# Optimization experiments

Hardware: AMD Instinct MI355X
Metric: run time of the kernel (lower is better)

The kernel has to match this reference:

```python
import jax, jax.numpy as jnp
import numpy as np

DIM = 768
NUM_HEADS = 8
GROUPS = 2


def setup_inputs() -> dict:
    key = jax.random.key(0)
    ks = jax.random.split(key, 6)
    B, N, C = 8, 1024, DIM
    x = jax.random.normal(ks[0], (B, N, C), dtype=jnp.float32)
    # nn.Linear weights stored (out_features, in_features), applied as x @ W.T
    w_qkv = jax.random.normal(ks[1], (3 * C, C), dtype=jnp.float32) * 0.02
    g_dim = C // GROUPS
    w_g0 = jax.random.normal(ks[2], (3 * g_dim, g_dim), dtype=jnp.float32) * 0.02
    w_g1 = jax.random.normal(ks[3], (3 * g_dim, g_dim), dtype=jnp.float32) * 0.02
    w_proj = jax.random.normal(ks[4], (C, C), dtype=jnp.float32) * 0.02
    b_proj = jax.random.normal(ks[5], (C,), dtype=jnp.float32) * 0.02
    return {"x": x, "w_qkv": w_qkv, "w_g0": w_g0, "w_g1": w_g1,
            "w_proj": w_proj, "b_proj": b_proj}


def reference(x, w_qkv, w_g0, w_g1, w_proj, b_proj):
    B, N, C = x.shape
    H = NUM_HEADS
    hd = C // H
    scale = hd ** (-0.5)  # qk_scale=None -> head_dim^-0.5, reused in group attn
    g = GROUPS
    g_dim = C // g

    # ---- standard MHSA branch ----
    qkv = (x @ w_qkv.T).reshape(B, N, 3, H, hd)
    qkv = jnp.transpose(qkv, (2, 0, 3, 1, 4))  # (3, B, H, N, hd)
    q, k, v = qkv[0], qkv[1], qkv[2]
    attn = jax.nn.softmax(jnp.einsum('bhnd,bhmd->bhnm', q, k) * scale, axis=-1)
    origin = jnp.einsum('bhnm,bhmd->bhnd', attn, v)  # (B, H, N, hd)
    origin = origin.swapaxes(1, 2).reshape(B, N, g, g_dim)

    # ---- sequential per-group head-fusion branch ----
    xg = x.reshape(B, N, g, g_dim)
    head_x = jnp.zeros((B, N, g_dim), dtype=x.dtype)
    outputs = []
    for i, w in enumerate([w_g0, w_g1]):  # fixed small loop, g=2
        cur = xg[:, :, i] + head_x
        qkv2 = (cur @ w.T).reshape(B, N, 3, g_dim)
        q2, k2, v2 = qkv2[:, :, 0], qkv2[:, :, 1], qkv2[:, :, 2]
        a2 = jax.nn.softmax(jnp.einsum('bnd,bmd->bnm', q2, k2) * scale, axis=-1)
        head_x = jnp.einsum('bnm,bmd->bnd', a2, v2)
        outputs.append(head_x + origin[:, :, i])

    out = jnp.concatenate(outputs, axis=-1)
    return out @ w_proj.T + b_proj
```

## Files before the change

### kernel.cpp

```cpp
#include <hip/hip_runtime.h>
#include <cstdint>
#include <cstddef>

#define DEV_INLINE __device__ __forceinline__

typedef __bf16 bf16;
typedef __bf16 bf16x8 __attribute__((ext_vector_type(8)));
typedef float f32x4 __attribute__((ext_vector_type(4)));

static constexpr int Bb = 8;
static constexpr int Nn = 1024;
static constexpr int Cc = 768;
static constexpr int HD = 96;
static constexpr int GD = 384;
#define SCALE_ 0.1020620726159658f

DEV_INLINE void gload_lds16(void* lds, const void* g) {
  __builtin_amdgcn_global_load_lds(
      (__attribute__((address_space(1))) void*)(void*)g,
      (__attribute__((address_space(3))) void*)lds, 16, 0, 0);
}

__global__ void k_f32_to_bf16(const float* __restrict__ src, bf16* __restrict__ dst, int n) {
  int i = (blockIdx.x * 256 + threadIdx.x) * 8;
  if (i >= n) return;
  float4 a = *(const float4*)(src + i);
  float4 b = *(const float4*)(src + i + 4);
  bf16x8 o;
  o[0] = (bf16)a.x; o[1] = (bf16)a.y; o[2] = (bf16)a.z; o[3] = (bf16)a.w;
  o[4] = (bf16)b.x; o[5] = (bf16)b.y; o[6] = (bf16)b.z; o[7] = (bf16)b.w;
  *(bf16x8*)(dst + i) = o;
}

__global__ void k_make_cur(const float* __restrict__ x, const float* __restrict__ hx,
                           bf16* __restrict__ cur, int gi) {
  int t = blockIdx.x * 256 + threadIdx.x;
  int m = t / 48;
  int d0 = (t % 48) * 8;
  const float* xr = x + (size_t)m * Cc + gi * GD + d0;
  float4 a = *(const float4*)xr;
  float4 b = *(const float4*)(xr + 4);
  if (gi) {
    const float* hr = hx + (size_t)m * GD + d0;
    float4 c = *(const float4*)hr;
    float4 d = *(const float4*)(hr + 4);
    a.x += c.x; a.y += c.y; a.z += c.z; a.w += c.w;
    b.x += d.x; b.y += d.y; b.z += d.z; b.w += d.w;
  }
  bf16x8 o;
  o[0] = (bf16)a.x; o[1] = (bf16)a.y; o[2] = (bf16)a.z; o[3] = (bf16)a.w;
  o[4] = (bf16)b.x; o[5] = (bf16)b.y; o[6] = (bf16)b.z; o[7] = (bf16)b.w;
  *(bf16x8*)(cur + (size_t)m * GD + d0) = o;
}

template <int EPI>
__global__ __launch_bounds__(256, 2)
void k_gemm(const bf16* __restrict__ A, const bf16* __restrict__ W, int K,
            int aZ, int wZ,
            bf16* __restrict__ o0, bf16* __restrict__ o1, bf16* __restrict__ o2,
            float* __restrict__ f0, const float* __restrict__ bias,
            const float* __restrict__ origin, int gi) {
  const int bm = blockIdx.x, bn = blockIdx.y, bz = blockIdx.z;
  const int tid = threadIdx.x;
  const int wave = tid >> 6, lane = tid & 63;
  const int wr = wave >> 1, wc = wave & 1;
  const int l15 = lane & 15, l4 = lane >> 4;

  A += (size_t)bz * aZ;
  W += (size_t)bz * wZ;

  __shared__ bf16 As[128 * 32];
  __shared__ bf16 Bs[128 * 32];

  f32x4 acc[4][4] = {};

  const int t8 = tid * 8;
  const int r0 = t8 >> 5, c0 = t8 & 31;
  const int r1 = r0 + 64;
  const bf16* Arow0 = A + (size_t)(bm * 128 + r0) * K + c0;
  const bf16* Arow1 = A + (size_t)(bm * 128 + r1) * K + c0;
  const bf16* Brow0 = W + (size_t)(bn * 128 + r0) * K + c0;
  const bf16* Brow1 = W + (size_t)(bn * 128 + r1) * K + c0;
  bf16* sA0 = &As[wave * 512];
  bf16* sA1 = &As[2048 + wave * 512];
  bf16* sB0 = &Bs[wave * 512];
  bf16* sB1 = &Bs[2048 + wave * 512];

  for (int k0 = 0; k0 < K; k0 += 32) {
    gload_lds16(sA0, Arow0 + k0);
    gload_lds16(sA1, Arow1 + k0);
    gload_lds16(sB0, Brow0 + k0);
    gload_lds16(sB1, Brow1 + k0);
    __syncthreads();
    bf16x8 af[4], bfr[4];
#pragma unroll
    for (int i = 0; i < 4; ++i) {
      af[i]  = *(const bf16x8*)&As[(wr * 64 + i * 16 + l15) * 32 + l4 * 8];
      bfr[i] = *(const bf16x8*)&Bs[(wc * 64 + i * 16 + l15) * 32 + l4 * 8];
    }
#pragma unroll
    for (int i = 0; i < 4; ++i)
#pragma unroll
      for (int j = 0; j < 4; ++j)
        acc[i][j] = __builtin_amdgcn_mfma_f32_16x16x32_bf16(af[i], bfr[j], acc[i][j], 0, 0, 0);
    __syncthreads();
  }

#pragma unroll
  for (int i = 0; i < 4; ++i) {
    const int mbase = bm * 128 + wr * 64 + i * 16 + l4 * 4;
#pragma unroll
    for (int j = 0; j < 4; ++j) {
      const int col = bn * 128 + wc * 64 + j * 16 + l15;
#pragma unroll
      for (int r = 0; r < 4; ++r) {
        const int row = mbase + r;
        const float val = acc[i][j][r];
        if constexpr (EPI == 2) {
          f0[(size_t)row * 768 + col] = val + bias[col];
        } else if constexpr (EPI == 3) {
          o0[((size_t)bz * 1024 + row) * 1024 + col] = (bf16)(val * SCALE_);
        } else if constexpr (EPI == 4) {
          const size_t gr = (size_t)bz * 1024 + row;
          f0[gr * 384 + col] = val;
          const size_t ci = gr * 768 + gi * 384 + col;
          o1[ci] = (bf16)(val + origin[ci]);
        } else if constexpr (EPI == 0) {
          const int bb = row >> 10, n = row & 1023;
          const int sct = col / 768, rem = col % 768;
          const int hh = rem / 96, dd = rem % 96;
          const bf16 bv = (bf16)val;
          if (sct == 0)      o0[((size_t)(bb * 8 + hh) * 1024 + n) * 96 + dd] = bv;
          else if (sct == 1) o1[((size_t)(bb * 8 + hh) * 1024 + n) * 96 + dd] = bv;
          else               o2[((size_t)(bb * 8 + hh) * 96 + dd) * 1024 + n] = bv;
        } else {
          const int bb = row >> 10, n = row & 1023;
          const int sct = col / 384, dd = col % 384;
          const bf16 bv = (bf16)val;
          if (sct == 0)      o0[(size_t)row * 384 + dd] = bv;
          else if (sct == 1) o1[(size_t)row * 384 + dd] = bv;
          else               o2[((size_t)bb * 384 + dd) * 1024 + n] = bv;
        }
      }
    }
  }
}

__global__ __launch_bounds__(256)
void k_softmax_rows(bf16* __restrict__ SP) {
  const int row = blockIdx.x * 4 + (threadIdx.x >> 6);
  const int lane = threadIdx.x & 63;
  bf16* R = SP + (size_t)row * 1024 + lane * 16;
  bf16x8 a = *(const bf16x8*)R;
  bf16x8 b = *(const bf16x8*)(R + 8);
  float v[16];
#pragma unroll
  for (int i = 0; i < 8; ++i) { v[i] = (float)a[i]; v[8 + i] = (float)b[i]; }
  float mx = -1e30f;
#pragma unroll
  for (int i = 0; i < 16; ++i) mx = fmaxf(mx, v[i]);
  mx = fmaxf(mx, __shfl_xor(mx, 1));
  mx = fmaxf(mx, __shfl_xor(mx, 2));
  mx = fmaxf(mx, __shfl_xor(mx, 4));
  mx = fmaxf(mx, __shfl_xor(mx, 8));
  mx = fmaxf(mx, __shfl_xor(mx, 16));
  mx = fmaxf(mx, __shfl_xor(mx, 32));
  float s = 0.f;
#pragma unroll
  for (int i = 0; i < 16; ++i) { v[i] = __expf(v[i] - mx); s += v[i]; }
  s += __shfl_xor(s, 1);
  s += __shfl_xor(s, 2);
  s += __shfl_xor(s, 4);
  s += __shfl_xor(s, 8);
  s += __shfl_xor(s, 16);
  s += __shfl_xor(s, 32);
  const float inv = 1.f / s;
#pragma unroll
  for (int i = 0; i < 8; ++i) { a[i] = (bf16)(v[i] * inv); b[i] = (bf16)(v[8 + i] * inv); }
  *(bf16x8*)R = a;
  *(bf16x8*)(R + 8) = b;
}

__global__ __launch_bounds__(256, 2)
void k_flash_mha(const bf16* __restrict__ Q, const bf16* __restrict__ Kt,
                 const bf16* __restrict__ Vt, float* __restrict__ origin) {
  const int bh = blockIdx.x, qb = blockIdx.y;
  const int b = bh >> 3, h = bh & 7;
  const int wave = threadIdx.x >> 6, lane = threadIdx.x & 63;
  const int l15 = lane & 15, l4 = lane >> 4;
  const bf16* Qh = Q + (size_t)bh * Nn * HD;
  const bf16* Kh = Kt + (size_t)bh * Nn * HD;
  const bf16* Vh = Vt + (size_t)bh * HD * Nn;
  const int q0 = qb * 128 + wave * 32;

  bf16x8 qf[2][3];
#pragma unroll
  for (int mf = 0; mf < 2; ++mf)
#pragma unroll
    for (int kf = 0; kf < 3; ++kf)
      qf[mf][kf] = *(const bf16x8*)&Qh[(size_t)(q0 + mf * 16 + l15) * HD + kf * 32 + l4 * 8];

  f32x4 o[2][6] = {};
  float mrow[2][4], lrow[2][4];
#pragma unroll
  for (int mf = 0; mf < 2; ++mf)
#pragma unroll
    for (int r = 0; r < 4; ++r) { mrow[mf][r] = -1e30f; lrow[mf][r] = 0.f; }

  __shared__ bf16 Plds[4][32 * 88];
  bf16* Pl = &Plds[wave][0];

  for (int n0 = 0; n0 < Nn; n0 += 64) {
    f32x4 s[2][4] = {};
#pragma unroll
    for (int nf = 0; nf < 4; ++nf)
#pragma unroll
      for (int kf = 0; kf < 3; ++kf) {
        bf16x8 kfr = *(const bf16x8*)&Kh[(size_t)(n0 + nf * 16 + l15) * HD + kf * 32 + l4 * 8];
#pragma unroll
        for (int mf = 0; mf < 2; ++mf)
          s[mf][nf] = __builtin_amdgcn_mfma_f32_16x16x32_bf16(qf[mf][kf], kfr, s[mf][nf], 0, 0, 0);
      }
#pragma unroll
    for (int mf = 0; mf < 2; ++mf)
#pragma unroll
      for (int r = 0; r < 4; ++r) {
        float mx = -1e30f;
#pragma unroll
        for (int nf = 0; nf < 4; ++nf) {
          s[mf][nf][r] *= SCALE_;
          mx = fmaxf(mx, s[mf][nf][r]);
        }
        mx = fmaxf(mx, __shfl_xor(mx, 1));
        mx = fmaxf(mx, __shfl_xor(mx, 2));
        mx = fmaxf(mx, __shfl_xor(mx, 4));
        mx = fmaxf(mx, __shfl_xor(mx, 8));
        float mnew = fmaxf(mrow[mf][r], mx);
        float alpha = __expf(mrow[mf][r] - mnew);
        mrow[mf][r] = mnew;
        float ls = 0.f;
#pragma unroll
        for (int nf = 0; nf < 4; ++nf) {
          float p = __expf(s[mf][nf][r] - mnew);
          s[mf][nf][r] = p;
          ls += p;
        }
        ls += __shfl_xor(ls, 1); ls += __shfl_xor(ls, 2);
        ls += __shfl_xor(ls, 4); ls += __shfl_xor(ls, 8);
        lrow[mf][r] = lrow[mf][r] * alpha + ls;
#pragma unroll
        for (int df = 0; df < 6; ++df) o[mf][df][r] *= alpha;
      }
#pragma unroll
    for (int mf = 0; mf < 2; ++mf)
#pragma unroll
      for (int nf = 0; nf < 4; ++nf)
#pragma unroll
        for (int r = 0; r < 4; ++r)
          Pl[(mf * 16 + l4 * 4 + r) * 88 + nf * 16 + l15] = (bf16)s[mf][nf][r];
    bf16x8 pa[2][2];
#pragma unroll
    for (int mf = 0; mf < 2; ++mf)
#pragma unroll
      for (int kf2 = 0; kf2 < 2; ++kf2)
        pa[mf][kf2] = *(const bf16x8*)&Pl[(mf * 16 + l15) * 88 + kf2 * 32 + l4 * 8];
#pragma unroll
    for (int df = 0; df < 6; ++df)
#pragma unroll
      for (int kf2 = 0; kf2 < 2; ++kf2) {
        bf16x8 vf = *(const bf16x8*)&Vh[(size_t)(df * 16 + l15) * Nn + n0 + kf2 * 32 + l4 * 8];
#pragma unroll
        for (int mf = 0; mf < 2; ++mf)
          o[mf][df] = __builtin_amdgcn_mfma_f32_16x16x32_bf16(pa[mf][kf2], vf, o[mf][df], 0, 0, 0);
      }
  }

  float* Og = origin + (size_t)b * Nn * Cc + h * HD;
#pragma unroll
  for (int mf = 0; mf < 2; ++mf)
#pragma unroll
    for (int r = 0; r < 4; ++r) {
      const int row = q0 + mf * 16 + l4 * 4 + r;
      const float inv = 1.f / lrow[mf][r];
#pragma unroll
      for (int df = 0; df < 6; ++df)
        Og[(size_t)row * Cc + df * 16 + l15] = o[mf][df][r] * inv;
    }
}

extern "C" void kernel_launch(void* const* d_in, const int* in_sizes, int n_in,
                              void* d_out, int out_size, void* d_ws, size_t ws_size,
                              hipStream_t stream) {
  const float* x      = (const float*)d_in[0];
  const float* w_qkv  = (const float*)d_in[1];
  const float* w_g0   = (const float*)d_in[2];
  const float* w_g1   = (const float*)d_in[3];
  const float* w_proj = (const float*)d_in[4];
  const float* b_proj = (const float*)d_in[5];
  float* out = (float*)d_out;

  char* ws = (char*)d_ws;
  size_t off = 0;
  auto alloc = [&](size_t bytes) {
    char* p = ws + off;
    off += (bytes + 255) & ~(size_t)255;
    return p;
  };
  bf16* xb     = (bf16*)alloc((size_t)8192 * 768 * 2);
  bf16* wqkvb  = (bf16*)alloc((size_t)2304 * 768 * 2);
  bf16* wg0b   = (bf16*)alloc((size_t)1152 * 384 * 2);
  bf16* wg1b   = (bf16*)alloc((size_t)1152 * 384 * 2);
  bf16* wprojb = (bf16*)alloc((size_t)768 * 768 * 2);
  float* origin = (float*)alloc((size_t)8192 * 768 * 4);
  char* R = alloc((size_t)67108864);
  bf16* Qb = (bf16*)R;
  bf16* Kb = (bf16*)(R + 12582912);
  bf16* Vt = (bf16*)(R + 25165824);
  bf16* curb = (bf16*)R;
  bf16* q2   = (bf16*)(R + 6291456);
  bf16* k2   = (bf16*)(R + 12582912);
  bf16* v2t  = (bf16*)(R + 18874368);
  float* hx  = (float*)(R + 25165824);
  bf16* cat  = (bf16*)(R + 37748736);
  bf16* SP   = (bf16*)(R + 50331648);

  k_f32_to_bf16<<<dim3(3072), 256, 0, stream>>>(x, xb, 8192 * 768);
  k_f32_to_bf16<<<dim3(864), 256, 0, stream>>>(w_qkv, wqkvb, 2304 * 768);
  k_f32_to_bf16<<<dim3(216), 256, 0, stream>>>(w_g0, wg0b, 1152 * 384);
  k_f32_to_bf16<<<dim3(216), 256, 0, stream>>>(w_g1, wg1b, 1152 * 384);
  k_f32_to_bf16<<<dim3(288), 256, 0, stream>>>(w_proj, wprojb, 768 * 768);

  k_gemm<0><<<dim3(64, 18), 256, 0, stream>>>(xb, wqkvb, 768, 0, 0, Qb, Kb, Vt, nullptr, nullptr, nullptr, 0);
  k_flash_mha<<<dim3(64, 8), 256, 0, stream>>>(Qb, Kb, Vt, origin);

  for (int gi = 0; gi < 2; ++gi) {
    const bf16* wg = gi ? wg1b : wg0b;
    k_make_cur<<<dim3(1536), 256, 0, stream>>>(x, hx, curb, gi);
    k_gemm<1><<<dim3(64, 9), 256, 0, stream>>>(curb, wg, 384, 0, 0, q2, k2, v2t, nullptr, nullptr, nullptr, 0);
    k_gemm<3><<<dim3(8, 8, 8), 256, 0, stream>>>(q2, k2, 384, 1024 * 384, 1024 * 384,
                                                 SP, nullptr, nullptr, nullptr, nullptr, nullptr, 0);
    k_softmax_rows<<<dim3(2048), 256, 0, stream>>>(SP);
    k_gemm<4><<<dim3(8, 3, 8), 256, 0, stream>>>(SP, v2t, 1024, 1024 * 1024, 384 * 1024,
                                                 nullptr, cat, nullptr, hx, nullptr, origin, gi);
  }

  k_gemm<2><<<dim3(64, 6), 256, 0, stream>>>(cat, wprojb, 768, 0, 0, nullptr, nullptr, nullptr, out, b_proj, nullptr, 0);
}
```

Baseline: 448.8 us.

## Double-buffer K/V tiles in LDS for flash MHA and fuse conversion kernels

```diff
diff --git a/kernel.cpp b/kernel.cpp
--- a/kernel.cpp
+++ b/kernel.cpp
@@ -5,6 +5,7 @@
 #define DEV_INLINE __device__ __forceinline__
 
 typedef __bf16 bf16;
+typedef __bf16 bf16x4 __attribute__((ext_vector_type(4)));
 typedef __bf16 bf16x8 __attribute__((ext_vector_type(8)));
 typedef float f32x4 __attribute__((ext_vector_type(4)));
 
@@ -21,15 +22,25 @@
       (__attribute__((address_space(3))) void*)lds, 16, 0, 0);
 }
 
-__global__ void k_f32_to_bf16(const float* __restrict__ src, bf16* __restrict__ dst, int n) {
-  int i = (blockIdx.x * 256 + threadIdx.x) * 8;
-  if (i >= n) return;
-  float4 a = *(const float4*)(src + i);
-  float4 b = *(const float4*)(src + i + 4);
+__global__ void k_convert_all(const float* __restrict__ x, const float* __restrict__ wqkv,
+                              const float* __restrict__ wg0, const float* __restrict__ wg1,
+                              const float* __restrict__ wproj,
+                              bf16* __restrict__ xb, bf16* __restrict__ wqkvb,
+                              bf16* __restrict__ wg0b, bf16* __restrict__ wg1b,
+                              bf16* __restrict__ wprojb) {
+  const int i = (blockIdx.x * 256 + threadIdx.x) * 8;
+  const float* src; bf16* dst; int off;
+  if (i < 6291456)      { src = x;     dst = xb;     off = i; }
+  else if (i < 8060928) { src = wqkv;  dst = wqkvb;  off = i - 6291456; }
+  else if (i < 8503296) { src = wg0;   dst = wg0b;   off = i - 8060928; }
+  else if (i < 8945664) { src = wg1;   dst = wg1b;   off = i - 8503296; }
+  else                  { src = wproj; dst = wprojb; off = i - 8945664; }
+  float4 a = *(const float4*)(src + off);
+  float4 b = *(const float4*)(src + off + 4);
   bf16x8 o;
   o[0] = (bf16)a.x; o[1] = (bf16)a.y; o[2] = (bf16)a.z; o[3] = (bf16)a.w;
   o[4] = (bf16)b.x; o[5] = (bf16)b.y; o[6] = (bf16)b.z; o[7] = (bf16)b.w;
-  *(bf16x8*)(dst + i) = o;
+  *(bf16x8*)(dst + off) = o;
 }
 
 __global__ void k_make_cur(const float* __restrict__ x, const float* __restrict__ hx,
@@ -193,6 +204,13 @@
   const bf16* Vh = Vt + (size_t)bh * HD * Nn;
   const int q0 = qb * 128 + wave * 32;
 
+  __shared__ bf16 Ks[2][64 * 96];
+  __shared__ bf16 Vs[2][96 * 64];
+  __shared__ bf16 Plds[4][32 * 88];
+  __shared__ float aux[4][32];
+  bf16* Pl = &Plds[wave][0];
+  float* Ax = &aux[wave][0];
+
   bf16x8 qf[2][3];
 #pragma unroll
   for (int mf = 0; mf < 2; ++mf)
@@ -201,63 +219,101 @@
       qf[mf][kf] = *(const bf16x8*)&Qh[(size_t)(q0 + mf * 16 + l15) * HD + kf * 32 + l4 * 8];
 
   f32x4 o[2][6] = {};
-  float mrow[2][4], lrow[2][4];
-#pragma unroll
-  for (int mf = 0; mf < 2; ++mf)
-#pragma unroll
-    for (int r = 0; r < 4; ++r) { mrow[mf][r] = -1e30f; lrow[mf][r] = 0.f; }
-
-  __shared__ bf16 Plds[4][32 * 88];
-  bf16* Pl = &Plds[wave][0];
-
-  for (int n0 = 0; n0 < Nn; n0 += 64) {
+  float mrow[2] = {-1e30f, -1e30f}, lrow[2] = {0.f, 0.f};
+
+  auto stageK = [&](int buf, int n0) {
+#pragma unroll
+    for (int i = 0; i < 3; ++i) {
+      const int c = i * 4 + wave;
+      gload_lds16(&Ks[buf][c * 512], Kh + (size_t)n0 * 96 + c * 512 + lane * 8);
+    }
+  };
+  auto stageV = [&](int buf, int n0) {
+#pragma unroll
+    for (int i = 0; i < 3; ++i) {
+      const int c = i * 4 + wave;
+      const int L = (c * 64 + lane) * 16;
+      const int row = L >> 7;
+      const int colb = (L & 127) ^ ((row & 7) << 4);
+      gload_lds16(&Vs[buf][c * 512], Vh + (size_t)row * Nn + n0 + (colb >> 1));
+    }
+  };
+
+  auto compute = [&](int buf) {
     f32x4 s[2][4] = {};
 #pragma unroll
-    for (int nf = 0; nf < 4; ++nf)
-#pragma unroll
-      for (int kf = 0; kf < 3; ++kf) {
-        bf16x8 kfr = *(const bf16x8*)&Kh[(size_t)(n0 + nf * 16 + l15) * HD + kf * 32 + l4 * 8];
+    for (int nf = 0; nf < 4; ++nf) {
+      bf16x8 kfr[3];
+#pragma unroll
+      for (int kf = 0; kf < 3; ++kf)
+        kfr[kf] = *(const bf16x8*)&Ks[buf][(nf * 16 + l15) * 96 + kf * 32 + l4 * 8];
+#pragma unroll
+      for (int kf = 0; kf < 3; ++kf)
 #pragma unroll
         for (int mf = 0; mf < 2; ++mf)
-          s[mf][nf] = __builtin_amdgcn_mfma_f32_16x16x32_bf16(qf[mf][kf], kfr, s[mf][nf], 0, 0, 0);
-      }
-#pragma unroll
-    for (int mf = 0; mf < 2; ++mf)
-#pragma unroll
-      for (int r = 0; r < 4; ++r) {
-        float mx = -1e30f;
-#pragma unroll
-        for (int nf = 0; nf < 4; ++nf) {
+          s[mf][nf] = __builtin_amdgcn_mfma_f32_16x16x32_bf16(kfr[kf], qf[mf][kf], s[mf][nf], 0, 0, 0);
+    }
+    float pmax[2];
+#pragma unroll
+    for (int mf = 0; mf < 2; ++mf) {
+      float mx = -1e30f;
+#pragma unroll
+      for (int nf = 0; nf < 4; ++nf)
+#pragma unroll
+        for (int r = 0; r < 4; ++r) {
           s[mf][nf][r] *= SCALE_;
           mx = fmaxf(mx, s[mf][nf][r]);
         }
-        mx = fmaxf(mx, __shfl_xor(mx, 1));
-        mx = fmaxf(mx, __shfl_xor(mx, 2));
-        mx = fmaxf(mx, __shfl_xor(mx, 4));
-        mx = fmaxf(mx, __shfl_xor(mx, 8));
-        float mnew = fmaxf(mrow[mf][r], mx);
-        float alpha = __expf(mrow[mf][r] - mnew);
-        mrow[mf][r] = mnew;
-        float ls = 0.f;
-#pragma unroll
-        for (int nf = 0; nf < 4; ++nf) {
-          float p = __expf(s[mf][nf][r] - mnew);
+      mx = fmaxf(mx, __shfl_xor(mx, 16));
+      mx = fmaxf(mx, __shfl_xor(mx, 32));
+      pmax[mf] = mx;
+    }
+    const bool need = (pmax[0] > mrow[0] + 8.f) || (pmax[1] > mrow[1] + 8.f);
+    if (__any(need)) {
+#pragma unroll
+      for (int mf = 0; mf < 2; ++mf) {
+        const float mnew = fmaxf(mrow[mf], pmax[mf]);
+        const float alpha = __expf(mrow[mf] - mnew);
+        mrow[mf] = mnew;
+        lrow[mf] *= alpha;
+        if (l4 == 0) Ax[mf * 16 + l15] = alpha;
+      }
+      float ar[2][4];
+#pragma unroll
+      for (int mf = 0; mf < 2; ++mf)
+#pragma unroll
+        for (int r = 0; r < 4; ++r) ar[mf][r] = Ax[mf * 16 + l4 * 4 + r];
+#pragma unroll
+      for (int mf = 0; mf < 2; ++mf)
+#pragma unroll
+        for (int df = 0; df < 6; ++df)
+#pragma unroll
+          for (int r = 0; r < 4; ++r) o[mf][df][r] *= ar[mf][r];
+    }
+#pragma unroll
+    for (int mf = 0; mf < 2; ++mf) {
+      float ls = 0.f;
+#pragma unroll
+      for (int nf = 0; nf < 4; ++nf)
+#pragma unroll
+        for (int r = 0; r < 4; ++r) {
+          const float p = __expf(s[mf][nf][r] - mrow[mf]);
           s[mf][nf][r] = p;
           ls += p;
         }
-        ls += __shfl_xor(ls, 1); ls += __shfl_xor(ls, 2);
-        ls += __shfl_xor(ls, 4); ls += __shfl_xor(ls, 8);
-        lrow[mf][r] = lrow[mf][r] * alpha + ls;
-#pragma unroll
-        for (int df = 0; df < 6; ++df) o[mf][df][r] *= alpha;
+      ls += __shfl_xor(ls, 16);
+      ls += __shfl_xor(ls, 32);
+      lrow[mf] += ls;
+    }
+#pragma unroll
+    for (int mf = 0; mf < 2; ++mf)
+#pragma unroll
+      for (int nf = 0; nf < 4; ++nf) {
+        bf16x4 pk;
+        pk[0] = (bf16)s[mf][nf][0]; pk[1] = (bf16)s[mf][nf][1];
+        pk[2] = (bf16)s[mf][nf][2]; pk[3] = (bf16)s[mf][nf][3];
+        *(bf16x4*)&Pl[(mf * 16 + l15) * 88 + nf * 16 + l4 * 4] = pk;
       }
-#pragma unroll
-    for (int mf = 0; mf < 2; ++mf)
-#pragma unroll
-      for (int nf = 0; nf < 4; ++nf)
-#pragma unroll
-        for (int r = 0; r < 4; ++r)
-          Pl[(mf * 16 + l4 * 4 + r) * 88 + nf * 16 + l15] = (bf16)s[mf][nf][r];
     bf16x8 pa[2][2];
 #pragma unroll
     for (int mf = 0; mf < 2; ++mf)
@@ -265,26 +321,53 @@
       for (int kf2 = 0; kf2 < 2; ++kf2)
         pa[mf][kf2] = *(const bf16x8*)&Pl[(mf * 16 + l15) * 88 + kf2 * 32 + l4 * 8];
 #pragma unroll
-    for (int df = 0; df < 6; ++df)
+    for (int df = 0; df < 6; ++df) {
+      bf16x8 vfr[2];
 #pragma unroll
       for (int kf2 = 0; kf2 < 2; ++kf2) {
-        bf16x8 vf = *(const bf16x8*)&Vh[(size_t)(df * 16 + l15) * Nn + n0 + kf2 * 32 + l4 * 8];
+        const int row = df * 16 + l15;
+        const int addr = row * 128 + ((kf2 * 64 + l4 * 16) ^ ((row & 7) << 4));
+        vfr[kf2] = *(const bf16x8*)((const char*)&Vs[buf][0] + addr);
+      }
+#pragma unroll
+      for (int kf2 = 0; kf2 < 2; ++kf2)
 #pragma unroll
         for (int mf = 0; mf < 2; ++mf)
-          o[mf][df] = __builtin_amdgcn_mfma_f32_16x16x32_bf16(pa[mf][kf2], vf, o[mf][df], 0, 0, 0);
-      }
-  }
-
+          o[mf][df] = __builtin_amdgcn_mfma_f32_16x16x32_bf16(pa[mf][kf2], vfr[kf2], o[mf][df], 0, 0, 0);
+    }
+  };
+
+  stageK(0, 0);
+  stageV(0, 0);
+  __syncthreads();
+  int cur = 0;
+  for (int t = 0; t < 16; ++t) {
+    const int nn = (t < 15) ? (t + 1) * 64 : 15 * 64;
+    stageK(cur ^ 1, nn);
+    stageV(cur ^ 1, nn);
+    compute(cur);
+    __syncthreads();
+    cur ^= 1;
+  }
+
+  if (l4 == 0) {
+    Ax[l15] = lrow[0];
+    Ax[16 + l15] = lrow[1];
+  }
+  float linv[2][4];
+#pragma unroll
+  for (int mf = 0; mf < 2; ++mf)
+#pragma unroll
+    for (int r = 0; r < 4; ++r) linv[mf][r] = 1.f / Ax[mf * 16 + l4 * 4 + r];
   float* Og = origin + (size_t)b * Nn * Cc + h * HD;
 #pragma unroll
   for (int mf = 0; mf < 2; ++mf)
 #pragma unroll
     for (int r = 0; r < 4; ++r) {
       const int row = q0 + mf * 16 + l4 * 4 + r;
-      const float inv = 1.f / lrow[mf][r];
 #pragma unroll
       for (int df = 0; df < 6; ++df)
-        Og[(size_t)row * Cc + df * 16 + l15] = o[mf][df][r] * inv;
+        Og[(size_t)row * Cc + df * 16 + l15] = o[mf][df][r] * linv[mf][r];
     }
 }
 
@@ -324,11 +407,8 @@
   bf16* cat  = (bf16*)(R + 37748736);
   bf16* SP   = (bf16*)(R + 50331648);
 
-  k_f32_to_bf16<<<dim3(3072), 256, 0, stream>>>(x, xb, 8192 * 768);
-  k_f32_to_bf16<<<dim3(864), 256, 0, stream>>>(w_qkv, wqkvb, 2304 * 768);
-  k_f32_to_bf16<<<dim3(216), 256, 0, stream>>>(w_g0, wg0b, 1152 * 384);
-  k_f32_to_bf16<<<dim3(216), 256, 0, stream>>>(w_g1, wg1b, 1152 * 384);
-  k_f32_to_bf16<<<dim3(288), 256, 0, stream>>>(w_proj, wprojb, 768 * 768);
+  k_convert_all<<<dim3(4656), 256, 0, stream>>>(x, w_qkv, w_g0, w_g1, w_proj,
+                                                xb, wqkvb, wg0b, wg1b, wprojb);
 
   k_gemm<0><<<dim3(64, 18), 256, 0, stream>>>(xb, wqkvb, 768, 0, 0, Qb, Kb, Vt, nullptr, nullptr, nullptr, 0);
   k_flash_mha<<<dim3(64, 8), 256, 0, stream>>>(Qb, Kb, Vt, origin);
```

Result: faster. 361.9 us (-19.4%).
